# Kernel optimization log

Hardware: AMD Instinct MI355X
Metric: run time of the kernel (lower is better)

## Reference

```python
import jax, jax.numpy as jnp
import numpy as np
import math

B, N, D, H, O = 2, 1024, 256, 4, 8
DT, STEPS = 0.1, 5


def setup_inputs() -> dict:
    key = jax.random.key(0)
    ks = jax.random.split(key, 8)
    inv_d = 1.0 / math.sqrt(D)
    inv_ho = 1.0 / math.sqrt(H * O)
    return {
        "x": jax.random.normal(ks[0], (B, N, D), jnp.float32),
        "Wq": jax.random.normal(ks[1], (D, D), jnp.float32) * inv_d,
        "Wk": jax.random.normal(ks[2], (D, D), jnp.float32) * inv_d,
        "Wp": jax.random.normal(ks[3], (H * O, D), jnp.float32) * inv_d,
        "bp": jnp.zeros((H * O,), jnp.float32),
        "Wo": jax.random.normal(ks[4], (D, H * O), jnp.float32) * inv_ho,
        "bo": jnp.zeros((D,), jnp.float32),
        "omega": jax.random.normal(ks[5], (H, O), jnp.float32) * 0.1,
        "coupling_scale": jnp.asarray(1.0, jnp.float32),
    }


def reference(x, Wq, Wk, Wp, bp, Wo, bo, omega, coupling_scale):
    dk = D // H
    # attention coupling J_ij = softmax(q_i.k_j / sqrt(d_k))  -> (B,H,N,N)
    q = (x @ Wq.T).reshape(B, N, H, dk).transpose(0, 2, 1, 3)
    k = (x @ Wk.T).reshape(B, N, H, dk).transpose(0, 2, 1, 3)
    J = jax.nn.softmax(jnp.einsum('bhid,bhjd->bhij', q, k) / math.sqrt(dk), axis=-1)
    # initial phases (B,H,N,O)
    phases = (x @ Wp.T + bp).reshape(B, N, H, O).transpose(0, 2, 1, 3)
    om = omega[None, :, None, :]  # (1,H,1,O)

    def step(ph, _):
        # sum_j J_ij sin(phi_j - phi_i) = cos(phi_i)*(J@sin phi) - sin(phi_i)*(J@cos phi)
        s, c = jnp.sin(ph), jnp.cos(ph)
        coupling = c * jnp.einsum('bhij,bhjo->bhio', J, s) - s * jnp.einsum('bhij,bhjo->bhio', J, c)
        new = ph + DT * (om + coupling_scale * coupling)
        new = jnp.remainder(new + jnp.pi, 2 * jnp.pi) - jnp.pi
        return new, None

    phases, _ = jax.lax.scan(step, phases, None, length=STEPS)
    sig = jnp.cos(phases).transpose(0, 2, 1, 3).reshape(B, N, H * O)
    return sig @ Wo.T + bo
```

## Files before the change

### kernel.cpp

```cpp
#include <hip/hip_runtime.h>
#include <hip/hip_bf16.h>
#include <math.h>


#define NB 1024
#define NH 4
#define DD 256
#define NO 8
#define PI_F      3.14159265358979323846f
#define TWO_PI_F  6.28318530717958647692f
#define INV_2PI_F 0.15915494309189533577f

typedef __attribute__((ext_vector_type(8))) short bf16x8;
typedef __attribute__((ext_vector_type(4))) float f32x4;

__device__ __forceinline__ float b2f_u(unsigned short s) {
    union { unsigned u; float f; } x; x.u = ((unsigned)s) << 16; return x.f;
}
__device__ __forceinline__ unsigned short f2b(float f) {
    union { float f; unsigned u; } v; v.f = f;
    unsigned r = v.u + 0x7FFFu + ((v.u >> 16) & 1u);
    return (unsigned short)(r >> 16);
}
template<bool F32>
__device__ __forceinline__ uint4 load_pack8(const void* p, size_t off) {
    if (!F32) return *(const uint4*)((const unsigned short*)p + off);
    const float* fp = (const float*)p + off;
    float4 a = *(const float4*)fp;
    float4 b = *(const float4*)(fp + 4);
    uint4 r;
    r.x = (unsigned)f2b(a.x) | ((unsigned)f2b(a.y) << 16);
    r.y = (unsigned)f2b(a.z) | ((unsigned)f2b(a.w) << 16);
    r.z = (unsigned)f2b(b.x) | ((unsigned)f2b(b.y) << 16);
    r.w = (unsigned)f2b(b.z) | ((unsigned)f2b(b.w) << 16);
    return r;
}
__device__ __forceinline__ void load8_rt(int f32, const void* p, int i, float* f) {
    if (f32) {
        const float* fp = (const float*)p + i;
        float4 a = *(const float4*)fp;
        float4 b = *(const float4*)(fp + 4);
        f[0]=a.x; f[1]=a.y; f[2]=a.z; f[3]=a.w;
        f[4]=b.x; f[5]=b.y; f[6]=b.z; f[7]=b.w;
    } else {
        uint4 u = *(const uint4*)((const unsigned short*)p + i);
        f[0] = b2f_u(u.x & 0xFFFFu); f[1] = b2f_u(u.x >> 16);
        f[2] = b2f_u(u.y & 0xFFFFu); f[3] = b2f_u(u.y >> 16);
        f[4] = b2f_u(u.z & 0xFFFFu); f[5] = b2f_u(u.z >> 16);
        f[6] = b2f_u(u.w & 0xFFFFu); f[7] = b2f_u(u.w >> 16);
    }
}
__device__ __forceinline__ float read_cs_bf16(const void* p) {
    float vb = b2f_u(*(const unsigned short*)p);
    bool ok = isfinite(vb) && fabsf(vb) > 1e-30f && fabsf(vb) < 1e30f;
    if (ok) return vb;
    return *(const float*)p;
}
__device__ __forceinline__ int detect_inline(const unsigned short* x) {
    int l = threadIdx.x & 63;
    float a0 = fabsf(b2f_u(x[2 * l]));
    float a1 = fabsf(b2f_u(x[2 * (l + 64)]));
    unsigned long long b0 = __ballot(!(a0 >= 1e-10f && a0 <= 100.0f));
    unsigned long long b1 = __ballot(!(a1 >= 1e-10f && a1 <= 100.0f));
    return (__popcll(b0) + __popcll(b1)) > 16;
}

template<bool F32>
__device__ void projm_impl(
    const void* __restrict__ x, const void* __restrict__ Wq,
    const void* __restrict__ Wk, const void* __restrict__ Wp,
    const void* __restrict__ bp,
    unsigned short* __restrict__ Qb, unsigned short* __restrict__ Kb,
    float* __restrict__ PH, unsigned short* __restrict__ SC)
{
    __shared__ uint4 Xsh[64 * 32];
    __shared__ uint4 Wsh[64 * 32];
    const int tid = threadIdx.x;
    const int ftile = blockIdx.x % 9, itile = blockIdx.x / 9;
    const int i0 = itile * 64, f0 = ftile * 64;
    const int wave = tid >> 6, lane = tid & 63;
    const int n = lane & 15, quad = lane >> 4;

    #pragma unroll
    for (int g = 0; g < 8; g++) {
        int fidx = g * 256 + tid;
        int row = fidx >> 5, q = fidx & 31;
        int sw = (q & 24) | ((q ^ row) & 7);
        Xsh[row * 32 + sw] = load_pack8<F32>(x, (size_t)(i0 + row) * 256 + q * 8);
        int wr = f0 + row;
        uint4 wv = make_uint4(0, 0, 0, 0);
        if (wr < 256)      wv = load_pack8<F32>(Wq, (size_t)wr * 256 + q * 8);
        else if (wr < 512) wv = load_pack8<F32>(Wk, (size_t)(wr - 256) * 256 + q * 8);
        else if (wr < 544) wv = load_pack8<F32>(Wp, (size_t)(wr - 512) * 256 + q * 8);
        Wsh[row * 32 + sw] = wv;
    }
    __syncthreads();

    f32x4 acc[4];
    #pragma unroll
    for (int s = 0; s < 4; s++) acc[s] = (f32x4){0.f, 0.f, 0.f, 0.f};
    const int xrow = wave * 16 + n;
    #pragma unroll
    for (int s = 0; s < 8; s++) {
        int qc = s * 4 + quad;
        bf16x8 b = ((const bf16x8*)Xsh)[xrow * 32 + ((qc & 24) | ((qc ^ xrow) & 7))];
        #pragma unroll
        for (int sub = 0; sub < 4; sub++) {
            int wr = sub * 16 + n;
            bf16x8 a = ((const bf16x8*)Wsh)[wr * 32 + ((qc & 24) | ((qc ^ wr) & 7))];
            acc[sub] = __builtin_amdgcn_mfma_f32_16x16x32_bf16(a, b, acc[sub], 0, 0, 0);
        }
    }

    const int ig = i0 + wave * 16 + n;
    const int bb = ig >> 10, nr = ig & 1023;
    if (ftile < 4) {
        #pragma unroll
        for (int sub = 0; sub < 4; sub++) {
            int dd = sub * 16 + quad * 4;
            ushort4 v = make_ushort4(f2b(acc[sub][0] * 0.125f), f2b(acc[sub][1] * 0.125f),
                                     f2b(acc[sub][2] * 0.125f), f2b(acc[sub][3] * 0.125f));
            *(ushort4*)(Qb + ((size_t)((bb * NH + ftile) * NB + nr)) * 64 + dd) = v;
        }
    } else if (ftile < 8) {
        int h = ftile - 4;
        #pragma unroll
        for (int sub = 0; sub < 4; sub++) {
            int dd = sub * 16 + quad * 4;
            ushort4 v = make_ushort4(f2b(acc[sub][0]), f2b(acc[sub][1]),
                                     f2b(acc[sub][2]), f2b(acc[sub][3]));
            *(ushort4*)(Kb + ((size_t)((bb * NH + h) * NB + nr)) * 64 + dd) = v;
        }
    } else {
        #pragma unroll
        for (int sub = 0; sub < 2; sub++) {
            #pragma unroll
            for (int r = 0; r < 4; r++) {
                int fp = sub * 16 + quad * 4 + r;
                int h2 = fp >> 3, o = fp & 7;
                float bpv = F32 ? ((const float*)bp)[fp]
                                : b2f_u(((const unsigned short*)bp)[fp]);
                float v = acc[sub][r] + bpv;
                int bh = bb * NH + h2;
                PH[(size_t)bh * 8192 + o * 1024 + nr] = v;
                float sv, cv;
                __sincosf(v, &sv, &cv);
                SC[(size_t)(bh * 16 + o) * 1024 + nr]     = f2b(sv);
                SC[(size_t)(bh * 16 + 8 + o) * 1024 + nr] = f2b(cv);
            }
        }
    }
}

__global__ __launch_bounds__(256) void k_projm(
    const unsigned short* x, const void* Wq, const void* Wk, const void* Wp,
    const void* bp, unsigned short* Qb, unsigned short* Kb, float* PH,
    unsigned short* SC)
{
    if (detect_inline(x)) projm_impl<true >(x, Wq, Wk, Wp, bp, Qb, Kb, PH, SC);
    else                  projm_impl<false>(x, Wq, Wk, Wp, bp, Qb, Kb, PH, SC);
}

__global__ __launch_bounds__(256) void k_scores(
    const unsigned short* __restrict__ Qb, const unsigned short* __restrict__ Kb,
    unsigned short* __restrict__ U, float* __restrict__ R)
{
    __shared__ uint4 Ksh[512 * 8];
    __shared__ float redS[2][2][16];
    const int tid = threadIdx.x;
    const int bh  = blockIdx.x >> 5;
    const int wave = tid >> 6, lane = tid & 63;
    const int n = lane & 15, quad = lane >> 4;
    const int iw = wave >> 1, jw = wave & 1;
    const int i0 = (blockIdx.x & 31) * 32 + iw * 16;

    const unsigned short* qrow = Qb + ((size_t)(bh * NB) + i0 + n) * 64;
    bf16x8 bq0 = *(const bf16x8*)(qrow + quad * 8);
    bf16x8 bq1 = *(const bf16x8*)(qrow + 32 + quad * 8);

    float s = 0.f;
    unsigned short* urow = U + ((size_t)(bh * NB) + i0 + n) * NB;
    #pragma unroll 1
    for (int half = 0; half < 2; half++) {
        __syncthreads();
        const unsigned short* ksrc = Kb + ((size_t)(bh * NB) + half * 512) * 64;
        #pragma unroll
        for (int g = 0; g < 16; g++) {
            int fidx = g * 256 + tid;
            int rl = fidx >> 3, q = fidx & 7;
            Ksh[rl * 8 + (q ^ (rl & 7))] = *(const uint4*)(ksrc + fidx * 8);
        }
        __syncthreads();
        for (int t = 0; t < 16; t++) {
            int jt = jw * 16 + t;
            int rl = jt * 16 + n;
            bf16x8 a0 = ((const bf16x8*)Ksh)[rl * 8 + (quad ^ (n & 7))];
            bf16x8 a1 = ((const bf16x8*)Ksh)[rl * 8 + ((4 + quad) ^ (n & 7))];
            f32x4 acc = {0.f, 0.f, 0.f, 0.f};
            acc = __builtin_amdgcn_mfma_f32_16x16x32_bf16(a0, bq0, acc, 0, 0, 0);
            acc = __builtin_amdgcn_mfma_f32_16x16x32_bf16(a1, bq1, acc, 0, 0, 0);
            float u0 = __expf(acc[0]);
            float u1 = __expf(acc[1]);
            float u2 = __expf(acc[2]);
            float u3 = __expf(acc[3]);
            s += (u0 + u1) + (u2 + u3);
            *(ushort4*)(urow + half * 512 + jt * 16 + quad * 4)
                = make_ushort4(f2b(u0), f2b(u1), f2b(u2), f2b(u3));
        }
    }
    s += __shfl_xor(s, 16);
    s += __shfl_xor(s, 32);
    if (lane < 16) redS[iw][jw][lane] = s;
    __syncthreads();
    if (jw == 0 && lane < 16)
        R[bh * NB + i0 + lane] = 1.0f / (redS[iw][0][lane] + redS[iw][1][lane]);
}

__global__ __launch_bounds__(256) void k_step(
    const unsigned short* __restrict__ xraw,
    const unsigned short* __restrict__ U, const float* __restrict__ R,
    const float* __restrict__ PHin, float* __restrict__ PHout,
    const unsigned short* __restrict__ SCin, unsigned short* __restrict__ SCout,
    const void* __restrict__ omega, const void* __restrict__ csp)
{
    __shared__ uint4 sc4[16 * 128];
    __shared__ f32x4 red[4][64];
    const int tid  = threadIdx.x;
    const int bh   = blockIdx.x >> 6;
    const int i0   = (blockIdx.x & 63) * 16;
    const int wave = tid >> 6, lane = tid & 63;
    const int n    = lane & 15, quad = lane >> 4;
    const int f32  = detect_inline(xraw);
    const float* phs = PHin + (size_t)bh * 8192;

    #pragma unroll
    for (int g = 0; g < 8; g++) {
        int fidx = g * 256 + tid;
        int row = fidx >> 7, col = fidx & 127;
        sc4[row * 128 + (col ^ (row & 7))]
            = *(const uint4*)(SCin + (size_t)(bh * 16 + row) * 1024 + col * 8);
    }
    __syncthreads();

    const unsigned short* urow = U + ((size_t)(bh * NB) + i0 + n) * NB;
    f32x4 acc = {0.f, 0.f, 0.f, 0.f};
    #pragma unroll
    for (int t = 0; t < 8; t++) {
        int it = wave * 8 + t;
        bf16x8 a = *(const bf16x8*)(urow + it * 32 + quad * 8);
        bf16x8 b = ((const bf16x8*)sc4)[n * 128 + ((it * 4 + quad) ^ (n & 7))];
        acc = __builtin_amdgcn_mfma_f32_16x16x32_bf16(a, b, acc, 0, 0, 0);
    }
    red[wave][lane] = acc;
    __syncthreads();

    if (wave == 0) {
        f32x4 a0 = red[0][lane], a1 = red[1][lane];
        f32x4 a2 = red[2][lane], a3 = red[3][lane];
        #pragma unroll
        for (int v = 0; v < 4; v++) acc[v] = (a0[v] + a1[v]) + (a2[v] + a3[v]);

        float C0 = __shfl_xor(acc[0], 8);
        float C1 = __shfl_xor(acc[1], 8);
        float C2 = __shfl_xor(acc[2], 8);
        float C3 = __shfl_xor(acc[3], 8);

        if (n < 8) {
            const int o = n, h = bh & 3;
            const float cs = f32 ? *(const float*)csp : read_cs_bf16(csp);
            const float om = f32 ? ((const float*)omega)[h * NO + o]
                                 : b2f_u(((const unsigned short*)omega)[h * NO + o]);
            float4 Rv = *(const float4*)(R + bh * NB + i0 + quad * 4);
            float4 pv = *(const float4*)(phs + o * 1024 + i0 + quad * 4);
            float S[4] = {acc[0], acc[1], acc[2], acc[3]};
            float C[4] = {C0, C1, C2, C3};
            float Rr[4] = {Rv.x, Rv.y, Rv.z, Rv.w};
            float P[4]  = {pv.x, pv.y, pv.z, pv.w};
            float op[4];
            #pragma unroll
            for (int r = 0; r < 4; r++) {
                float si, ci;
                __sincosf(P[r], &si, &ci);
                float coup = (ci * S[r] - si * C[r]) * Rr[r];
                float v = P[r] + 0.1f * (om + cs * coup);
                float t2 = v + PI_F;
                t2 -= floorf(t2 * INV_2PI_F) * TWO_PI_F;
                op[r] = t2 - PI_F;
            }
            *(float4*)(PHout + (size_t)bh * 8192 + o * 1024 + i0 + quad * 4)
                = make_float4(op[0], op[1], op[2], op[3]);
            #pragma unroll
            for (int r = 0; r < 4; r++) {
                float sn, cn;
                __sincosf(op[r], &sn, &cn);
                int i = i0 + quad * 4 + r;
                SCout[(size_t)(bh * 16 + o) * 1024 + i]     = f2b(sn);
                SCout[(size_t)(bh * 16 + 8 + o) * 1024 + i] = f2b(cn);
            }
        }
    }
}

__global__ __launch_bounds__(256) void k_out(
    const unsigned short* __restrict__ xraw,
    const unsigned short* __restrict__ SC,
    const void* __restrict__ Wo, const void* __restrict__ bo,
    void* __restrict__ out)
{
    __shared__ float sig[32];
    const int tid = threadIdx.x;
    const int b = blockIdx.x >> 10, n = blockIdx.x & 1023;
    const int f32 = detect_inline(xraw);
    if (tid < 32) {
        int h = tid >> 3, o = tid & 7;
        sig[tid] = b2f_u(SC[(size_t)((b * NH + h) * 16 + 8 + o) * 1024 + n]);
    }
    __syncthreads();
    float acc = f32 ? ((const float*)bo)[tid] : b2f_u(((const unsigned short*)bo)[tid]);
    #pragma unroll
    for (int d0 = 0; d0 < 32; d0 += 8) {
        float w[8];
        load8_rt(f32, Wo, tid * 32 + d0, w);
        #pragma unroll
        for (int t = 0; t < 8; t++) acc += sig[d0 + t] * w[t];
    }
    size_t oi = (size_t)blockIdx.x * DD + tid;
    if (f32) ((float*)out)[oi] = acc;
    else     ((unsigned short*)out)[oi] = f2b(acc);
}

extern "C" void kernel_launch(void* const* d_in, const int* in_sizes, int n_in,
                              void* d_out, int out_size, void* d_ws, size_t ws_size,
                              hipStream_t stream)
{
    const unsigned short* x = (const unsigned short*)d_in[0];
    const void* Wq  = d_in[1];
    const void* Wk  = d_in[2];
    const void* Wp  = d_in[3];
    const void* bp  = d_in[4];
    const void* Wo  = d_in[5];
    const void* bo  = d_in[6];
    const void* om  = d_in[7];
    const void* cs  = d_in[8];

    char* w = (char*)d_ws;
    unsigned short* Qb  = (unsigned short*)w;
    unsigned short* Kb  = (unsigned short*)(w + (1u << 20));
    float*          R   = (float*)(w + (2u << 20));
    float*          PH0 = (float*)(w + (2u << 20) + (64u << 10));
    float*          PH1 = (float*)(w + (2u << 20) + (320u << 10));
    unsigned short* SC0 = (unsigned short*)(w + (2u << 20) + (576u << 10));
    unsigned short* SC1 = (unsigned short*)(w + (2u << 20) + (832u << 10));
    unsigned short* U   = (unsigned short*)(w + (2u << 20) + (1088u << 10));

    k_projm <<<288, 256, 0, stream>>>(x, Wq, Wk, Wp, bp, Qb, Kb, PH0, SC0);
    k_scores<<<256, 256, 0, stream>>>(Qb, Kb, U, R);
    k_step<<<512, 256, 0, stream>>>(x, U, R, PH0, PH1, SC0, SC1, om, cs);
    k_step<<<512, 256, 0, stream>>>(x, U, R, PH1, PH0, SC1, SC0, om, cs);
    k_step<<<512, 256, 0, stream>>>(x, U, R, PH0, PH1, SC0, SC1, om, cs);
    k_step<<<512, 256, 0, stream>>>(x, U, R, PH1, PH0, SC1, SC0, om, cs);
    k_step<<<512, 256, 0, stream>>>(x, U, R, PH0, PH1, SC0, SC1, om, cs);
    k_out<<<2048, 256, 0, stream>>>(x, SC1, Wo, bo, d_out);
}
```

Measured before the change: 140.7 us.

## Drop LDS staging in scores and step kernels, read operands directly from global

```diff
diff --git a/kernel.cpp b/kernel.cpp
--- a/kernel.cpp
+++ b/kernel.cpp
@@ -165,14 +165,12 @@
     const unsigned short* __restrict__ Qb, const unsigned short* __restrict__ Kb,
     unsigned short* __restrict__ U, float* __restrict__ R)
 {
-    __shared__ uint4 Ksh[512 * 8];
-    __shared__ float redS[2][2][16];
+    __shared__ float redS[4][16];
     const int tid = threadIdx.x;
-    const int bh  = blockIdx.x >> 5;
+    const int bh  = blockIdx.x >> 6;
+    const int i0  = (blockIdx.x & 63) * 16;
     const int wave = tid >> 6, lane = tid & 63;
     const int n = lane & 15, quad = lane >> 4;
-    const int iw = wave >> 1, jw = wave & 1;
-    const int i0 = (blockIdx.x & 31) * 32 + iw * 16;
 
     const unsigned short* qrow = Qb + ((size_t)(bh * NB) + i0 + n) * 64;
     bf16x8 bq0 = *(const bf16x8*)(qrow + quad * 8);
@@ -180,40 +178,31 @@
 
     float s = 0.f;
     unsigned short* urow = U + ((size_t)(bh * NB) + i0 + n) * NB;
-    #pragma unroll 1
-    for (int half = 0; half < 2; half++) {
-        __syncthreads();
-        const unsigned short* ksrc = Kb + ((size_t)(bh * NB) + half * 512) * 64;
-        #pragma unroll
-        for (int g = 0; g < 16; g++) {
-            int fidx = g * 256 + tid;
-            int rl = fidx >> 3, q = fidx & 7;
-            Ksh[rl * 8 + (q ^ (rl & 7))] = *(const uint4*)(ksrc + fidx * 8);
-        }
-        __syncthreads();
-        for (int t = 0; t < 16; t++) {
-            int jt = jw * 16 + t;
-            int rl = jt * 16 + n;
-            bf16x8 a0 = ((const bf16x8*)Ksh)[rl * 8 + (quad ^ (n & 7))];
-            bf16x8 a1 = ((const bf16x8*)Ksh)[rl * 8 + ((4 + quad) ^ (n & 7))];
-            f32x4 acc = {0.f, 0.f, 0.f, 0.f};
-            acc = __builtin_amdgcn_mfma_f32_16x16x32_bf16(a0, bq0, acc, 0, 0, 0);
-            acc = __builtin_amdgcn_mfma_f32_16x16x32_bf16(a1, bq1, acc, 0, 0, 0);
-            float u0 = __expf(acc[0]);
-            float u1 = __expf(acc[1]);
-            float u2 = __expf(acc[2]);
-            float u3 = __expf(acc[3]);
-            s += (u0 + u1) + (u2 + u3);
-            *(ushort4*)(urow + half * 512 + jt * 16 + quad * 4)
-                = make_ushort4(f2b(u0), f2b(u1), f2b(u2), f2b(u3));
-        }
+    const unsigned short* kbase = Kb + ((size_t)(bh * NB) + n) * 64;
+    #pragma unroll 2
+    for (int t = 0; t < 16; t++) {
+        int jt = wave * 16 + t;
+        const unsigned short* arow = kbase + (size_t)jt * 16 * 64;
+        bf16x8 a0 = *(const bf16x8*)(arow + quad * 8);
+        bf16x8 a1 = *(const bf16x8*)(arow + 32 + quad * 8);
+        f32x4 acc = {0.f, 0.f, 0.f, 0.f};
+        acc = __builtin_amdgcn_mfma_f32_16x16x32_bf16(a0, bq0, acc, 0, 0, 0);
+        acc = __builtin_amdgcn_mfma_f32_16x16x32_bf16(a1, bq1, acc, 0, 0, 0);
+        float u0 = __expf(acc[0]);
+        float u1 = __expf(acc[1]);
+        float u2 = __expf(acc[2]);
+        float u3 = __expf(acc[3]);
+        s += (u0 + u1) + (u2 + u3);
+        *(ushort4*)(urow + jt * 16 + quad * 4)
+            = make_ushort4(f2b(u0), f2b(u1), f2b(u2), f2b(u3));
     }
     s += __shfl_xor(s, 16);
     s += __shfl_xor(s, 32);
-    if (lane < 16) redS[iw][jw][lane] = s;
+    if (lane < 16) redS[wave][lane] = s;
     __syncthreads();
-    if (jw == 0 && lane < 16)
-        R[bh * NB + i0 + lane] = 1.0f / (redS[iw][0][lane] + redS[iw][1][lane]);
+    if (wave == 0 && lane < 16)
+        R[bh * NB + i0 + lane]
+            = 1.0f / (redS[0][lane] + redS[1][lane] + redS[2][lane] + redS[3][lane]);
 }
 
 __global__ __launch_bounds__(256) void k_step(
@@ -223,7 +212,6 @@
     const unsigned short* __restrict__ SCin, unsigned short* __restrict__ SCout,
     const void* __restrict__ omega, const void* __restrict__ csp)
 {
-    __shared__ uint4 sc4[16 * 128];
     __shared__ f32x4 red[4][64];
     const int tid  = threadIdx.x;
     const int bh   = blockIdx.x >> 6;
@@ -233,22 +221,14 @@
     const int f32  = detect_inline(xraw);
     const float* phs = PHin + (size_t)bh * 8192;
 
-    #pragma unroll
-    for (int g = 0; g < 8; g++) {
-        int fidx = g * 256 + tid;
-        int row = fidx >> 7, col = fidx & 127;
-        sc4[row * 128 + (col ^ (row & 7))]
-            = *(const uint4*)(SCin + (size_t)(bh * 16 + row) * 1024 + col * 8);
-    }
-    __syncthreads();
-
-    const unsigned short* urow = U + ((size_t)(bh * NB) + i0 + n) * NB;
+    const unsigned short* urow  = U + ((size_t)(bh * NB) + i0 + n) * NB;
+    const unsigned short* scrow = SCin + (size_t)(bh * 16 + n) * 1024;
     f32x4 acc = {0.f, 0.f, 0.f, 0.f};
     #pragma unroll
     for (int t = 0; t < 8; t++) {
         int it = wave * 8 + t;
-        bf16x8 a = *(const bf16x8*)(urow + it * 32 + quad * 8);
-        bf16x8 b = ((const bf16x8*)sc4)[n * 128 + ((it * 4 + quad) ^ (n & 7))];
+        bf16x8 a = *(const bf16x8*)(urow  + it * 32 + quad * 8);
+        bf16x8 b = *(const bf16x8*)(scrow + it * 32 + quad * 8);
         acc = __builtin_amdgcn_mfma_f32_16x16x32_bf16(a, b, acc, 0, 0, 0);
     }
     red[wave][lane] = acc;
@@ -354,7 +334,7 @@
     unsigned short* U   = (unsigned short*)(w + (2u << 20) + (1088u << 10));
 
     k_projm <<<288, 256, 0, stream>>>(x, Wq, Wk, Wp, bp, Qb, Kb, PH0, SC0);
-    k_scores<<<256, 256, 0, stream>>>(Qb, Kb, U, R);
+    k_scores<<<512, 256, 0, stream>>>(Qb, Kb, U, R);
     k_step<<<512, 256, 0, stream>>>(x, U, R, PH0, PH1, SC0, SC1, om, cs);
     k_step<<<512, 256, 0, stream>>>(x, U, R, PH1, PH0, SC1, SC0, om, cs);
     k_step<<<512, 256, 0, stream>>>(x, U, R, PH0, PH1, SC0, SC1, om, cs);
```

Measured after the change: 142.6 us. About the same (+1.4%).
